# Performance work log

Measured on AMD Instinct MI355X. Metric: run time of the kernel, lower is better.

The kernel has to match this reference:

```python
import jax, jax.numpy as jnp
import numpy as np

B, S, HID, H = 2, 2048, 1024, 16
D_HEAD = HID // H  # 64
EPS = 1e-5


def _gammas():
    lo, hi = np.log(1.0 / 512.0), np.log(1.0 / 32.0)
    return (1.0 - np.exp(np.linspace(lo, hi, H))).astype(np.float32)


def _decay_mask():
    # D[h, n, m] = gamma_h^(n-m) for n >= m else 0  (causal exponential decay)
    gam = jnp.asarray(_gammas())                      # [H]
    pos = jnp.arange(S, dtype=jnp.float32)
    diff = pos[:, None] - pos[None, :]                # [S, S]
    keep = diff >= 0
    logg = jnp.log(gam)[:, None, None]                # [H,1,1]
    safe = jnp.where(keep, diff, 0.0)[None]           # avoid inf for masked entries
    return jnp.where(keep[None], jnp.exp(safe * logg), 0.0)  # [H, S, S]


def setup_inputs() -> dict:
    key = jax.random.key(0)
    ks = jax.random.split(key, 10)
    rn = lambda k, shape, s=1.0: jax.random.normal(k, shape, dtype=jnp.float32) * s
    return {
        "x": rn(ks[0], (B, S, HID)),
        "wq": rn(ks[1], (H, D_HEAD, D_HEAD), 1.0 / np.sqrt(D_HEAD)),
        "bq": rn(ks[2], (H, D_HEAD), 0.02),
        "wk": rn(ks[3], (H, D_HEAD, D_HEAD), 1.0 / np.sqrt(D_HEAD)),
        "bk": rn(ks[4], (H, D_HEAD), 0.02),
        "wv": rn(ks[5], (H, D_HEAD, D_HEAD), 1.0 / np.sqrt(D_HEAD)),
        "theta": rn(ks[6], (H, D_HEAD), 1.0 / D_HEAD),
        "gn_weight": jnp.ones((HID,), jnp.float32),
        "gn_bias": jnp.zeros((HID,), jnp.float32),
        "weight1": rn(ks[7], (HID, HID), 1.0 / HID),
        "weight2": rn(ks[8], (HID, HID), 1.0 / HID),
    }


def reference(x, wq, bq, wk, bk, wv, theta, gn_weight, gn_bias, weight1, weight2):
    # Per-head retention (all heads vectorized; torch loops over heads).
    xh = x.reshape(B, S, H, D_HEAD)
    q = jnp.einsum('bshd,hde->bshe', xh, wq) + bq
    k = jnp.einsum('bshd,hde->bshe', xh, wk) + bk
    v = jnp.einsum('bshd,hde->bshe', xh, wv)
    # Complex rotary factors exp(i*n*theta) on q, conj on k -> real part of q k^H:
    ang = jnp.arange(S, dtype=jnp.float32)[:, None, None] * theta[None]  # [S,H,d]
    cs, sn = jnp.cos(ang), jnp.sin(ang)
    scores = (jnp.einsum('bshd,bthd->bhst', q * cs, k * cs)
              + jnp.einsum('bshd,bthd->bhst', q * sn, k * sn))  # Re(QK^H) [B,H,S,S]
    scores = scores * _decay_mask()[None]                        # decay mask
    ret = jnp.einsum('bhst,bthd->bshd', scores, v)               # [B,S,H,d]
    # GroupNorm with groups = n_heads over channels (per-head normalization).
    mean = jnp.mean(ret, axis=-1, keepdims=True)
    var = jnp.var(ret, axis=-1, keepdims=True)
    retn = (ret - mean) * jax.lax.rsqrt(var + EPS)
    retn = retn.reshape(B, S, HID) * gn_weight + gn_bias
    # Swish gate on x @ W1, residual add, project with W2.
    gate = x @ weight1
    out = gate * jax.nn.sigmoid(gate) + retn
    return out @ weight2
```

## Files before the change

kernel.cpp:

```cpp
#include <hip/hip_runtime.h>
#include <cstdint>
#include <cstddef>

#define B_ 2
#define S_ 2048
#define HID_ 1024
#define H_ 16
#define DH_ 64

typedef __attribute__((ext_vector_type(8))) short short8;
typedef __attribute__((ext_vector_type(8))) unsigned short ushort8;
typedef __attribute__((ext_vector_type(4))) unsigned short ushort4v;
typedef __attribute__((ext_vector_type(4))) float floatx4;
typedef __attribute__((ext_vector_type(4))) float float4v;

static __device__ __forceinline__ unsigned short f2bf(float f) {
  unsigned int u = __float_as_uint(f);
  u += 0x7fffu + ((u >> 16) & 1u);
  return (unsigned short)(u >> 16);
}
static __device__ __forceinline__ float bf2f(unsigned short h) {
  return __uint_as_float(((unsigned int)h) << 16);
}

__global__ __launch_bounds__(256) void convert_kernel(
    const float* __restrict__ x, const float* __restrict__ w1,
    const float* __restrict__ w2, unsigned short* __restrict__ x_bf,
    unsigned short* __restrict__ w1t, unsigned short* __restrict__ w2t_hi,
    unsigned short* __restrict__ w2t_lo) {
  const int NX = B_ * S_ * HID_;
  const int NW = HID_ * HID_;
  int idx = blockIdx.x * 256 + threadIdx.x;
  if (idx < NX) {
    x_bf[idx] = f2bf(x[idx]);
  } else if (idx < NX + NW) {
    int i = idx - NX;
    int n = i >> 10, k = i & 1023;
    w1t[i] = f2bf(w1[k * HID_ + n]);
  } else if (idx < NX + 2 * NW) {
    int i = idx - NX - NW;
    int n = i >> 10, k = i & 1023;
    float v = w2[k * HID_ + n];
    unsigned short h = f2bf(v);
    w2t_hi[i] = h;
    w2t_lo[i] = f2bf(v - bf2f(h));
  }
}

__global__ __launch_bounds__(256) void qkv_kernel(
    const float* __restrict__ x, const float* __restrict__ wq,
    const float* __restrict__ bq, const float* __restrict__ wk,
    const float* __restrict__ bk, const float* __restrict__ wv,
    const float* __restrict__ theta, float* __restrict__ q_f,
    unsigned short* __restrict__ k_h, unsigned short* __restrict__ k_l,
    unsigned short* __restrict__ v_th, unsigned short* __restrict__ v_tl,
    int b) {
  __shared__ __align__(16) float xs[64 * 68];
  __shared__ __align__(16) float wqs[64 * 68];
  __shared__ __align__(16) float wks[64 * 68];
  __shared__ __align__(16) float wvs[64 * 68];

  int tid = threadIdx.x;
  int st = blockIdx.x, h = blockIdx.y;
  int s0 = st * 64;

#pragma unroll
  for (int i = 0; i < 4; ++i) {
    int cid = tid + i * 256;
    int r = cid >> 4, c4 = (cid & 15) * 4;
    *reinterpret_cast<float4v*>(&xs[r * 68 + c4]) =
        *reinterpret_cast<const float4v*>(x + ((size_t)(b * S_ + s0 + r)) * HID_ + h * DH_ + c4);
  }
#pragma unroll
  for (int i = 0; i < 4; ++i) {
    int cid = tid + i * 256;
    int d = cid >> 4, c4 = (cid & 15) * 4;
    *reinterpret_cast<float4v*>(&wqs[d * 68 + c4]) =
        *reinterpret_cast<const float4v*>(wq + (size_t)(h * DH_ + d) * DH_ + c4);
    *reinterpret_cast<float4v*>(&wks[d * 68 + c4]) =
        *reinterpret_cast<const float4v*>(wk + (size_t)(h * DH_ + d) * DH_ + c4);
    *reinterpret_cast<float4v*>(&wvs[d * 68 + c4]) =
        *reinterpret_cast<const float4v*>(wv + (size_t)(h * DH_ + d) * DH_ + c4);
  }
  __syncthreads();

  int rg = tid >> 3;
  int cg = tid & 7;
  int r0 = rg * 2, c0 = cg * 8;

  float aq[2][8], ak[2][8], av[2][8];
#pragma unroll
  for (int i = 0; i < 2; ++i)
#pragma unroll
    for (int j = 0; j < 8; ++j) { aq[i][j] = 0.f; ak[i][j] = 0.f; av[i][j] = 0.f; }

  for (int d = 0; d < 64; ++d) {
    float x0 = xs[(r0 + 0) * 68 + d];
    float x1 = xs[(r0 + 1) * 68 + d];
#pragma unroll
    for (int j = 0; j < 8; ++j) {
      float wqv = wqs[d * 68 + c0 + j];
      float wkv = wks[d * 68 + c0 + j];
      float wvv = wvs[d * 68 + c0 + j];
      aq[0][j] += x0 * wqv; aq[1][j] += x1 * wqv;
      ak[0][j] += x0 * wkv; ak[1][j] += x1 * wkv;
      av[0][j] += x0 * wvv; av[1][j] += x1 * wvv;
    }
  }

  float thv[8], bqv[8], bkv[8];
#pragma unroll
  for (int j = 0; j < 8; ++j) {
    thv[j] = theta[h * DH_ + c0 + j];
    bqv[j] = bq[h * DH_ + c0 + j];
    bkv[j] = bk[h * DH_ + c0 + j];
  }

  __syncthreads();
  unsigned short* VtH = reinterpret_cast<unsigned short*>(xs);
  unsigned short* VtL = reinterpret_cast<unsigned short*>(wqs);

#pragma unroll
  for (int i = 0; i < 2; ++i) {
    int s = s0 + r0 + i;
    size_t qb = ((size_t)h * S_ + s) * 128;
    ushort8 kch, kcl, ksh, ksl;
#pragma unroll
    for (int j = 0; j < 8; ++j) {
      float q = aq[i][j] + bqv[j];
      float k = ak[i][j] + bkv[j];
      float ang = (float)s * thv[j];
      float cs = cosf(ang), sn = sinf(ang);
      q_f[qb + c0 + j] = q * cs;
      q_f[qb + 64 + c0 + j] = q * sn;
      float kc = k * cs, ksn = k * sn;
      unsigned short h1 = f2bf(kc);
      kch[j] = h1;
      kcl[j] = f2bf(kc - bf2f(h1));
      unsigned short h2 = f2bf(ksn);
      ksh[j] = h2;
      ksl[j] = f2bf(ksn - bf2f(h2));
      float vv = av[i][j];
      unsigned short vh1 = f2bf(vv);
      VtH[(c0 + j) * 72 + (r0 + i)] = vh1;
      VtL[(c0 + j) * 72 + (r0 + i)] = f2bf(vv - bf2f(vh1));
    }
    *reinterpret_cast<ushort8*>(k_h + qb + c0) = kch;
    *reinterpret_cast<ushort8*>(k_h + qb + 64 + c0) = ksh;
    *reinterpret_cast<ushort8*>(k_l + qb + c0) = kcl;
    *reinterpret_cast<ushort8*>(k_l + qb + 64 + c0) = ksl;
  }
  __syncthreads();
#pragma unroll
  for (int i = 0; i < 2; ++i) {
    int cid = tid + i * 256;
    int d = cid >> 3, t8 = (cid & 7) * 8;
    size_t gb = ((size_t)(h * 64 + d)) * S_ + s0 + t8;
    *reinterpret_cast<ushort8*>(v_th + gb) = *reinterpret_cast<const ushort8*>(&VtH[d * 72 + t8]);
    *reinterpret_cast<ushort8*>(v_tl + gb) = *reinterpret_cast<const ushort8*>(&VtL[d * 72 + t8]);
  }
}

__global__ __launch_bounds__(256) void retention_fold_kernel(
    const float* __restrict__ q_f, const unsigned short* __restrict__ k_h,
    const unsigned short* __restrict__ k_l,
    const unsigned short* __restrict__ v_th,
    const unsigned short* __restrict__ v_tl, const float* __restrict__ gn_w,
    const float* __restrict__ gn_b, float* __restrict__ retn, int b) {
  __shared__ __align__(16) unsigned short Kh[2][64 * 136];
  __shared__ __align__(16) unsigned short Kl[2][64 * 136];
  __shared__ __align__(16) unsigned short Vh[2][64 * 72];
  __shared__ __align__(16) unsigned short Vl[2][64 * 72];
  __shared__ __align__(16) float Sc[64 * 68];
  __shared__ float gnred[64][8];

  int tid = threadIdx.x;
  int w = tid >> 6;
  int lane = tid & 63, ln = lane & 15, quad = lane >> 4;
  int qp = blockIdx.x, h = blockIdx.y;
  int prow = quad * 4;

  const float lo_c = -6.2383246250395075f, hi_c = -3.4657359027997265f;
  float gam = 1.f - __expf(lo_c + (hi_c - lo_c) * ((float)h * (1.f / 15.f)));
  float logg = __logf(gam);

  float rowf[4], colf[4];
#pragma unroll
  for (int rr = 0; rr < 4; ++rr)
    rowf[rr] = __expf((float)(w * 16 + prow + rr) * logg);
#pragma unroll
  for (int ns = 0; ns < 4; ++ns)
    colf[ns] = __expf(-(float)(ns * 16 + ln) * logg);

  const unsigned short* khb = k_h + (size_t)h * S_ * 128;
  const unsigned short* klb = k_l + (size_t)h * S_ * 128;
  const unsigned short* vhb = v_th + (size_t)h * 64 * S_;
  const unsigned short* vlb = v_tl + (size_t)h * 64 * S_;

  for (int pass = 0; pass < 2; ++pass) {
    int qt = pass ? (31 - qp) : qp;
    int s0 = qt * 64;

    int sQ = s0 + w * 16 + ln;
    const float* qrow = q_f + ((size_t)h * S_ + sQ) * 128 + quad * 8;
    short8 qh[4], ql[4];
#pragma unroll
    for (int c = 0; c < 4; ++c) {
#pragma unroll
      for (int j = 0; j < 8; ++j) {
        float qv = qrow[c * 32 + j];
        unsigned short hh = f2bf(qv);
        qh[c][j] = (short)hh;
        ql[c][j] = (short)f2bf(qv - bf2f(hh));
      }
    }

    floatx4 accO[4];
#pragma unroll
    for (int i = 0; i < 4; ++i) accO[i] = (floatx4){0.f, 0.f, 0.f, 0.f};

    __syncthreads();
#pragma unroll
    for (int i = 0; i < 4; ++i) {
      int cid = tid + i * 256;
      int r = cid >> 4, c8 = (cid & 15) * 8;
      *reinterpret_cast<ushort8*>(&Kh[0][r * 136 + c8]) =
          *reinterpret_cast<const ushort8*>(khb + (size_t)r * 128 + c8);
      *reinterpret_cast<ushort8*>(&Kl[0][r * 136 + c8]) =
          *reinterpret_cast<const ushort8*>(klb + (size_t)r * 128 + c8);
    }
#pragma unroll
    for (int i = 0; i < 2; ++i) {
      int cid = tid + i * 256;
      int d = cid >> 3, t8 = (cid & 7) * 8;
      *reinterpret_cast<ushort8*>(&Vh[0][d * 72 + t8]) =
          *reinterpret_cast<const ushort8*>(vhb + (size_t)d * S_ + t8);
      *reinterpret_cast<ushort8*>(&Vl[0][d * 72 + t8]) =
          *reinterpret_cast<const ushort8*>(vlb + (size_t)d * S_ + t8);
    }

    for (int kt = 0; kt <= qt; ++kt) {
      int cur = kt & 1;
      __syncthreads();

      ushort8 skh[4], skl[4], svh[2], svl[2];
      if (kt < qt) {
        int t0n = (kt + 1) * 64;
#pragma unroll
        for (int i = 0; i < 4; ++i) {
          int cid = tid + i * 256;
          int r = cid >> 4, c8 = (cid & 15) * 8;
          skh[i] = *reinterpret_cast<const ushort8*>(khb + ((size_t)(t0n + r)) * 128 + c8);
          skl[i] = *reinterpret_cast<const ushort8*>(klb + ((size_t)(t0n + r)) * 128 + c8);
        }
#pragma unroll
        for (int i = 0; i < 2; ++i) {
          int cid = tid + i * 256;
          int d = cid >> 3, t8 = (cid & 7) * 8;
          svh[i] = *reinterpret_cast<const ushort8*>(vhb + (size_t)d * S_ + t0n + t8);
          svl[i] = *reinterpret_cast<const ushort8*>(vlb + (size_t)d * S_ + t0n + t8);
        }
      }

      floatx4 accS[4];
#pragma unroll
      for (int ns = 0; ns < 4; ++ns) {
        floatx4 a = (floatx4){0.f, 0.f, 0.f, 0.f};
#pragma unroll
        for (int ks = 0; ks < 4; ++ks) {
          int off = (ns * 16 + ln) * 136 + ks * 32 + quad * 8;
          short8 kh = *reinterpret_cast<const short8*>(&Kh[cur][off]);
          short8 kl = *reinterpret_cast<const short8*>(&Kl[cur][off]);
          a = __builtin_amdgcn_mfma_f32_16x16x32_bf16(qh[ks], kh, a, 0, 0, 0);
          a = __builtin_amdgcn_mfma_f32_16x16x32_bf16(ql[ks], kh, a, 0, 0, 0);
          a = __builtin_amdgcn_mfma_f32_16x16x32_bf16(qh[ks], kl, a, 0, 0, 0);
        }
        accS[ns] = a;
      }

      float tf = __expf((float)(64 * (qt - kt)) * logg);
      float trf[4];
#pragma unroll
      for (int rr = 0; rr < 4; ++rr) trf[rr] = tf * rowf[rr];
      if (kt < qt) {
#pragma unroll
        for (int ns = 0; ns < 4; ++ns)
#pragma unroll
          for (int rr = 0; rr < 4; ++rr)
            Sc[(w * 16 + prow + rr) * 68 + ns * 16 + ln] =
                accS[ns][rr] * trf[rr] * colf[ns];
      } else {
#pragma unroll
        for (int ns = 0; ns < 4; ++ns) {
          int col = ns * 16 + ln;
#pragma unroll
          for (int rr = 0; rr < 4; ++rr) {
            int row = w * 16 + prow + rr;
            float v = accS[ns][rr] * trf[rr] * colf[ns];
            Sc[row * 68 + col] = (row >= col) ? v : 0.f;
          }
        }
      }

      if (kt < qt) {
        int nx = cur ^ 1;
#pragma unroll
        for (int i = 0; i < 4; ++i) {
          int cid = tid + i * 256;
          int r = cid >> 4, c8 = (cid & 15) * 8;
          *reinterpret_cast<ushort8*>(&Kh[nx][r * 136 + c8]) = skh[i];
          *reinterpret_cast<ushort8*>(&Kl[nx][r * 136 + c8]) = skl[i];
        }
#pragma unroll
        for (int i = 0; i < 2; ++i) {
          int cid = tid + i * 256;
          int d = cid >> 3, t8 = (cid & 7) * 8;
          *reinterpret_cast<ushort8*>(&Vh[nx][d * 72 + t8]) = svh[i];
          *reinterpret_cast<ushort8*>(&Vl[nx][d * 72 + t8]) = svl[i];
        }
      }

#pragma unroll
      for (int ks = 0; ks < 2; ++ks) {
        const float* prow_p = &Sc[(w * 16 + ln) * 68 + ks * 32 + quad * 8];
        short8 ph, pl;
#pragma unroll
        for (int j = 0; j < 8; ++j) {
          float pv = prow_p[j];
          unsigned short hh = f2bf(pv);
          ph[j] = (short)hh;
          pl[j] = (short)f2bf(pv - bf2f(hh));
        }
#pragma unroll
        for (int ds = 0; ds < 4; ++ds) {
          int voff = (ds * 16 + ln) * 72 + ks * 32 + quad * 8;
          short8 vh = *reinterpret_cast<const short8*>(&Vh[cur][voff]);
          short8 vl = *reinterpret_cast<const short8*>(&Vl[cur][voff]);
          accO[ds] = __builtin_amdgcn_mfma_f32_16x16x32_bf16(ph, vh, accO[ds], 0, 0, 0);
          accO[ds] = __builtin_amdgcn_mfma_f32_16x16x32_bf16(pl, vh, accO[ds], 0, 0, 0);
          accO[ds] = __builtin_amdgcn_mfma_f32_16x16x32_bf16(ph, vl, accO[ds], 0, 0, 0);
        }
      }
    }

#pragma unroll
    for (int ds = 0; ds < 4; ++ds)
#pragma unroll
      for (int rr = 0; rr < 4; ++rr)
        Sc[(w * 16 + quad * 4 + rr) * 68 + ds * 16 + ln] = accO[ds][rr];

    int r2 = tid >> 2;
    int sub = tid & 3;
    float a16[16];
#pragma unroll
    for (int i = 0; i < 16; ++i) a16[i] = Sc[r2 * 68 + sub * 16 + i];

    float psum = 0.f, psq = 0.f;
#pragma unroll
    for (int i = 0; i < 16; ++i) { psum += a16[i]; psq += a16[i] * a16[i]; }
    gnred[r2][sub] = psum;
    gnred[r2][4 + sub] = psq;
    float sum = gnred[r2][0] + gnred[r2][1] + gnred[r2][2] + gnred[r2][3];
    float sq = gnred[r2][4] + gnred[r2][5] + gnred[r2][6] + gnred[r2][7];
    float mean = sum * (1.f / 64.f);
    float var = sq * (1.f / 64.f) - mean * mean;
    float rstd = rsqrtf(var + 1e-5f);

    size_t obase = ((size_t)(b * S_ + s0 + r2)) * HID_ + h * DH_ + sub * 16;
#pragma unroll
    for (int i = 0; i < 16; ++i) {
      float gw = gn_w[h * DH_ + sub * 16 + i];
      float gb = gn_b[h * DH_ + sub * 16 + i];
      retn[obase + i] = (a16[i] - mean) * rstd * gw + gb;
    }
  }
}

__global__ __launch_bounds__(256) void gemm_gate_kernel(
    const unsigned short* __restrict__ A, const unsigned short* __restrict__ Bt,
    const float* __restrict__ retn, unsigned short* __restrict__ pre_hi,
    unsigned short* __restrict__ pre_lo) {
  const int K = HID_;
  __shared__ __align__(16) unsigned short Al[128 * 56];
  __shared__ __align__(16) unsigned short Bl[128 * 56];

  int tid = threadIdx.x;
  int lane = tid & 63, ln = lane & 15, quad = lane >> 4;
  int w = tid >> 6, wm = w >> 1, wn = w & 1;
  int m0 = blockIdx.y * 128, n0 = blockIdx.x * 128;

  floatx4 acc[4][4];
#pragma unroll
  for (int i = 0; i < 4; ++i)
#pragma unroll
    for (int j = 0; j < 4; ++j) acc[i][j] = (floatx4){0.f, 0.f, 0.f, 0.f};

  for (int k0 = 0; k0 < K; k0 += 32) {
    __syncthreads();
#pragma unroll
    for (int i = 0; i < 2; ++i) {
      int cid = tid + i * 256;
      int r = cid >> 2, c8 = (cid & 3) * 8;
      *reinterpret_cast<ushort8*>(&Al[r * 56 + c8]) =
          *reinterpret_cast<const ushort8*>(A + (size_t)(m0 + r) * K + k0 + c8);
      *reinterpret_cast<ushort8*>(&Bl[r * 56 + c8]) =
          *reinterpret_cast<const ushort8*>(Bt + (size_t)(n0 + r) * K + k0 + c8);
    }
    __syncthreads();

    short8 af[4], bfr[4];
#pragma unroll
    for (int i = 0; i < 4; ++i) {
      af[i] = *reinterpret_cast<const short8*>(&Al[(wm * 64 + i * 16 + ln) * 56 + quad * 8]);
      bfr[i] = *reinterpret_cast<const short8*>(&Bl[(wn * 64 + i * 16 + ln) * 56 + quad * 8]);
    }
#pragma unroll
    for (int mi = 0; mi < 4; ++mi)
#pragma unroll
      for (int ni = 0; ni < 4; ++ni)
        acc[mi][ni] = __builtin_amdgcn_mfma_f32_16x16x32_bf16(af[mi], bfr[ni], acc[mi][ni], 0, 0, 0);
  }

#pragma unroll
  for (int mi = 0; mi < 4; ++mi) {
#pragma unroll
    for (int r = 0; r < 4; ++r) {
      int row = m0 + wm * 64 + mi * 16 + quad * 4 + r;
#pragma unroll
      for (int ni = 0; ni < 4; ++ni) {
        int col = n0 + wn * 64 + ni * 16 + ln;
        float g = acc[mi][ni][r];
        float val = g * (1.f / (1.f + __expf(-g))) + retn[(size_t)row * HID_ + col];
        unsigned short hh = f2bf(val);
        size_t oidx = (size_t)row * HID_ + col;
        pre_hi[oidx] = hh;
        pre_lo[oidx] = f2bf(val - bf2f(hh));
      }
    }
  }
}

__global__ __launch_bounds__(256) void gemm_out_kernel(
    const unsigned short* __restrict__ Ah, const unsigned short* __restrict__ Alo,
    const unsigned short* __restrict__ Bth, const unsigned short* __restrict__ Btlo,
    float* __restrict__ out_f) {
  const int K = HID_;
  __shared__ __align__(16) unsigned short AhS[128 * 56];
  __shared__ __align__(16) unsigned short AlS[128 * 56];
  __shared__ __align__(16) unsigned short BhS[128 * 56];
  __shared__ __align__(16) unsigned short BlS[128 * 56];

  int tid = threadIdx.x;
  int lane = tid & 63, ln = lane & 15, quad = lane >> 4;
  int w = tid >> 6, wm = w >> 1, wn = w & 1;
  int m0 = blockIdx.y * 128, n0 = blockIdx.x * 128;

  floatx4 acc[4][4];
#pragma unroll
  for (int i = 0; i < 4; ++i)
#pragma unroll
    for (int j = 0; j < 4; ++j) acc[i][j] = (floatx4){0.f, 0.f, 0.f, 0.f};

  for (int k0 = 0; k0 < K; k0 += 32) {
    __syncthreads();
#pragma unroll
    for (int i = 0; i < 2; ++i) {
      int cid = tid + i * 256;
      int r = cid >> 2, c8 = (cid & 3) * 8;
      size_t ga = (size_t)(m0 + r) * K + k0 + c8;
      size_t gb = (size_t)(n0 + r) * K + k0 + c8;
      *reinterpret_cast<ushort8*>(&AhS[r * 56 + c8]) = *reinterpret_cast<const ushort8*>(Ah + ga);
      *reinterpret_cast<ushort8*>(&AlS[r * 56 + c8]) = *reinterpret_cast<const ushort8*>(Alo + ga);
      *reinterpret_cast<ushort8*>(&BhS[r * 56 + c8]) = *reinterpret_cast<const ushort8*>(Bth + gb);
      *reinterpret_cast<ushort8*>(&BlS[r * 56 + c8]) = *reinterpret_cast<const ushort8*>(Btlo + gb);
    }
    __syncthreads();

    short8 afh[4], afl[4], bfh[4], bfl[4];
#pragma unroll
    for (int i = 0; i < 4; ++i) {
      int ao = (wm * 64 + i * 16 + ln) * 56 + quad * 8;
      int bo = (wn * 64 + i * 16 + ln) * 56 + quad * 8;
      afh[i] = *reinterpret_cast<const short8*>(&AhS[ao]);
      afl[i] = *reinterpret_cast<const short8*>(&AlS[ao]);
      bfh[i] = *reinterpret_cast<const short8*>(&BhS[bo]);
      bfl[i] = *reinterpret_cast<const short8*>(&BlS[bo]);
    }
#pragma unroll
    for (int mi = 0; mi < 4; ++mi)
#pragma unroll
      for (int ni = 0; ni < 4; ++ni) {
        floatx4 a = acc[mi][ni];
        a = __builtin_amdgcn_mfma_f32_16x16x32_bf16(afh[mi], bfh[ni], a, 0, 0, 0);
        a = __builtin_amdgcn_mfma_f32_16x16x32_bf16(afl[mi], bfh[ni], a, 0, 0, 0);
        a = __builtin_amdgcn_mfma_f32_16x16x32_bf16(afh[mi], bfl[ni], a, 0, 0, 0);
        acc[mi][ni] = a;
      }
  }

#pragma unroll
  for (int mi = 0; mi < 4; ++mi) {
#pragma unroll
    for (int r = 0; r < 4; ++r) {
      int row = m0 + wm * 64 + mi * 16 + quad * 4 + r;
#pragma unroll
      for (int ni = 0; ni < 4; ++ni) {
        int col = n0 + wn * 64 + ni * 16 + ln;
        out_f[(size_t)row * HID_ + col] = acc[mi][ni][r];
      }
    }
  }
}

extern "C" void kernel_launch(void* const* d_in, const int* in_sizes, int n_in,
                              void* d_out, int out_size, void* d_ws,
                              size_t ws_size, hipStream_t stream) {
  (void)in_sizes; (void)n_in; (void)out_size; (void)ws_size;
  const float* x = (const float*)d_in[0];
  const float* wq = (const float*)d_in[1];
  const float* bq = (const float*)d_in[2];
  const float* wk = (const float*)d_in[3];
  const float* bk = (const float*)d_in[4];
  const float* wv = (const float*)d_in[5];
  const float* theta = (const float*)d_in[6];
  const float* gn_w = (const float*)d_in[7];
  const float* gn_b = (const float*)d_in[8];
  const float* w1 = (const float*)d_in[9];
  const float* w2 = (const float*)d_in[10];

  const size_t MB = 1024 * 1024;
  char* ws = (char*)d_ws;
  unsigned short* x_bf   = (unsigned short*)(ws + 0 * MB);
  unsigned short* w1t    = (unsigned short*)(ws + 8 * MB);
  unsigned short* w2t_hi = (unsigned short*)(ws + 10 * MB);
  unsigned short* w2t_lo = (unsigned short*)(ws + 12 * MB);
  float*          q_f    = (float*)(ws + 14 * MB);
  unsigned short* k_h    = (unsigned short*)(ws + 30 * MB);
  unsigned short* k_l    = (unsigned short*)(ws + 38 * MB);
  unsigned short* v_th   = (unsigned short*)(ws + 46 * MB);
  unsigned short* v_tl   = (unsigned short*)(ws + 50 * MB);
  float*          retn   = (float*)(ws + 54 * MB);
  unsigned short* pre_hi = (unsigned short*)(ws + 14 * MB);
  unsigned short* pre_lo = (unsigned short*)(ws + 22 * MB);
  float* out = (float*)d_out;

  convert_kernel<<<dim3(24576), 256, 0, stream>>>(x, w1, w2, x_bf, w1t, w2t_hi, w2t_lo);
  for (int b = 0; b < B_; ++b) {
    qkv_kernel<<<dim3(S_ / 64, H_), 256, 0, stream>>>(
        x, wq, bq, wk, bk, wv, theta, q_f, k_h, k_l, v_th, v_tl, b);
    retention_fold_kernel<<<dim3(16, H_), 256, 0, stream>>>(
        q_f, k_h, k_l, v_th, v_tl, gn_w, gn_b, retn, b);
  }
  gemm_gate_kernel<<<dim3(HID_ / 128, (B_ * S_) / 128), 256, 0, stream>>>(
      x_bf, w1t, retn, pre_hi, pre_lo);
  gemm_out_kernel<<<dim3(HID_ / 128, (B_ * S_) / 128), 256, 0, stream>>>(
      pre_hi, pre_lo, w2t_hi, w2t_lo, out);
}
```

Baseline: 372.0 us.

## Pre-split Q into bf16 hi/lo, XOR-swizzle LDS tiles, remap retention grid

The qkv kernel now writes Q as bf16 hi/lo pairs, so the retention kernel no longer reads fp32 Q and splits it per element. The retention kernel's K, V and score tiles drop row padding in shared memory and use an XOR swizzle to avoid bank conflicts, with vectorized float4 reads of scores. The grid is flattened to 256 blocks and blockIdx is remapped so that heads are interleaved across blocks, which changes the order work is dispatched. The swizzle adds index arithmetic, and the Q workspace layout changes.

```diff
diff --git a/kernel.cpp b/kernel.cpp
--- a/kernel.cpp
+++ b/kernel.cpp
@@ -51,7 +51,8 @@
     const float* __restrict__ x, const float* __restrict__ wq,
     const float* __restrict__ bq, const float* __restrict__ wk,
     const float* __restrict__ bk, const float* __restrict__ wv,
-    const float* __restrict__ theta, float* __restrict__ q_f,
+    const float* __restrict__ theta,
+    unsigned short* __restrict__ q_h, unsigned short* __restrict__ q_l,
     unsigned short* __restrict__ k_h, unsigned short* __restrict__ k_l,
     unsigned short* __restrict__ v_th, unsigned short* __restrict__ v_tl,
     int b) {
@@ -124,15 +125,20 @@
   for (int i = 0; i < 2; ++i) {
     int s = s0 + r0 + i;
     size_t qb = ((size_t)h * S_ + s) * 128;
-    ushort8 kch, kcl, ksh, ksl;
+    ushort8 qch, qcl, qsh, qsl, kch, kcl, ksh, ksl;
 #pragma unroll
     for (int j = 0; j < 8; ++j) {
       float q = aq[i][j] + bqv[j];
       float k = ak[i][j] + bkv[j];
       float ang = (float)s * thv[j];
       float cs = cosf(ang), sn = sinf(ang);
-      q_f[qb + c0 + j] = q * cs;
-      q_f[qb + 64 + c0 + j] = q * sn;
+      float qc = q * cs, qs = q * sn;
+      unsigned short hq1 = f2bf(qc);
+      qch[j] = hq1;
+      qcl[j] = f2bf(qc - bf2f(hq1));
+      unsigned short hq2 = f2bf(qs);
+      qsh[j] = hq2;
+      qsl[j] = f2bf(qs - bf2f(hq2));
       float kc = k * cs, ksn = k * sn;
       unsigned short h1 = f2bf(kc);
       kch[j] = h1;
@@ -145,6 +151,10 @@
       VtH[(c0 + j) * 72 + (r0 + i)] = vh1;
       VtL[(c0 + j) * 72 + (r0 + i)] = f2bf(vv - bf2f(vh1));
     }
+    *reinterpret_cast<ushort8*>(q_h + qb + c0) = qch;
+    *reinterpret_cast<ushort8*>(q_h + qb + 64 + c0) = qsh;
+    *reinterpret_cast<ushort8*>(q_l + qb + c0) = qcl;
+    *reinterpret_cast<ushort8*>(q_l + qb + 64 + c0) = qsl;
     *reinterpret_cast<ushort8*>(k_h + qb + c0) = kch;
     *reinterpret_cast<ushort8*>(k_h + qb + 64 + c0) = ksh;
     *reinterpret_cast<ushort8*>(k_l + qb + c0) = kcl;
@@ -161,23 +171,35 @@
   }
 }
 
+#define KOFF(buf, row, cu) ((buf) * 16384 + (row) * 256 + ((((cu) * 2)) ^ (((row) & 7) << 4)))
+#define VOFF(buf, d, tu)   ((buf) * 8192 + (d) * 128 + ((((tu) * 2)) ^ (((d) & 7) << 4)))
+#define SCOFF(row, colb)   ((row) * 256 + ((colb) ^ (((row) & 7) << 4)))
+
 __global__ __launch_bounds__(256) void retention_fold_kernel(
-    const float* __restrict__ q_f, const unsigned short* __restrict__ k_h,
-    const unsigned short* __restrict__ k_l,
-    const unsigned short* __restrict__ v_th,
-    const unsigned short* __restrict__ v_tl, const float* __restrict__ gn_w,
-    const float* __restrict__ gn_b, float* __restrict__ retn, int b) {
-  __shared__ __align__(16) unsigned short Kh[2][64 * 136];
-  __shared__ __align__(16) unsigned short Kl[2][64 * 136];
-  __shared__ __align__(16) unsigned short Vh[2][64 * 72];
-  __shared__ __align__(16) unsigned short Vl[2][64 * 72];
-  __shared__ __align__(16) float Sc[64 * 68];
+    const unsigned short* __restrict__ q_h, const unsigned short* __restrict__ q_l,
+    const unsigned short* __restrict__ k_h, const unsigned short* __restrict__ k_l,
+    const unsigned short* __restrict__ v_th, const unsigned short* __restrict__ v_tl,
+    const float* __restrict__ gn_w, const float* __restrict__ gn_b,
+    float* __restrict__ retn, int b) {
+  __shared__ __align__(16) unsigned short Kh[2][64 * 128];
+  __shared__ __align__(16) unsigned short Kl[2][64 * 128];
+  __shared__ __align__(16) unsigned short Vh[2][64 * 64];
+  __shared__ __align__(16) unsigned short Vl[2][64 * 64];
+  __shared__ __align__(16) float Sc[64 * 64];
   __shared__ float gnred[64][8];
+
+  char* KhB = (char*)Kh;
+  char* KlB = (char*)Kl;
+  char* VhB = (char*)Vh;
+  char* VlB = (char*)Vl;
+  char* ScB = (char*)Sc;
 
   int tid = threadIdx.x;
   int w = tid >> 6;
   int lane = tid & 63, ln = lane & 15, quad = lane >> 4;
-  int qp = blockIdx.x, h = blockIdx.y;
+  int f = blockIdx.x;
+  int h = ((f & 7) << 1) | ((f >> 7) & 1);
+  int qp = (f >> 3) & 15;
   int prow = quad * 4;
 
   const float lo_c = -6.2383246250395075f, hi_c = -3.4657359027997265f;
@@ -202,17 +224,13 @@
     int s0 = qt * 64;
 
     int sQ = s0 + w * 16 + ln;
-    const float* qrow = q_f + ((size_t)h * S_ + sQ) * 128 + quad * 8;
-    short8 qh[4], ql[4];
+    const unsigned short* qhp = q_h + ((size_t)h * S_ + sQ) * 128 + quad * 8;
+    const unsigned short* qlp = q_l + ((size_t)h * S_ + sQ) * 128 + quad * 8;
+    short8 qfh[4], qfl[4];
 #pragma unroll
     for (int c = 0; c < 4; ++c) {
-#pragma unroll
-      for (int j = 0; j < 8; ++j) {
-        float qv = qrow[c * 32 + j];
-        unsigned short hh = f2bf(qv);
-        qh[c][j] = (short)hh;
-        ql[c][j] = (short)f2bf(qv - bf2f(hh));
-      }
+      qfh[c] = *reinterpret_cast<const short8*>(qhp + c * 32);
+      qfl[c] = *reinterpret_cast<const short8*>(qlp + c * 32);
     }
 
     floatx4 accO[4];
@@ -224,18 +242,20 @@
     for (int i = 0; i < 4; ++i) {
       int cid = tid + i * 256;
       int r = cid >> 4, c8 = (cid & 15) * 8;
-      *reinterpret_cast<ushort8*>(&Kh[0][r * 136 + c8]) =
+      int ko = KOFF(0, r, c8);
+      *reinterpret_cast<ushort8*>(KhB + ko) =
           *reinterpret_cast<const ushort8*>(khb + (size_t)r * 128 + c8);
-      *reinterpret_cast<ushort8*>(&Kl[0][r * 136 + c8]) =
+      *reinterpret_cast<ushort8*>(KlB + ko) =
           *reinterpret_cast<const ushort8*>(klb + (size_t)r * 128 + c8);
     }
 #pragma unroll
     for (int i = 0; i < 2; ++i) {
       int cid = tid + i * 256;
       int d = cid >> 3, t8 = (cid & 7) * 8;
-      *reinterpret_cast<ushort8*>(&Vh[0][d * 72 + t8]) =
+      int vo = VOFF(0, d, t8);
+      *reinterpret_cast<ushort8*>(VhB + vo) =
           *reinterpret_cast<const ushort8*>(vhb + (size_t)d * S_ + t8);
-      *reinterpret_cast<ushort8*>(&Vl[0][d * 72 + t8]) =
+      *reinterpret_cast<ushort8*>(VlB + vo) =
           *reinterpret_cast<const ushort8*>(vlb + (size_t)d * S_ + t8);
     }
 
@@ -266,14 +286,15 @@
 #pragma unroll
       for (int ns = 0; ns < 4; ++ns) {
         floatx4 a = (floatx4){0.f, 0.f, 0.f, 0.f};
+        int row = ns * 16 + ln;
 #pragma unroll
         for (int ks = 0; ks < 4; ++ks) {
-          int off = (ns * 16 + ln) * 136 + ks * 32 + quad * 8;
-          short8 kh = *reinterpret_cast<const short8*>(&Kh[cur][off]);
-          short8 kl = *reinterpret_cast<const short8*>(&Kl[cur][off]);
-          a = __builtin_amdgcn_mfma_f32_16x16x32_bf16(qh[ks], kh, a, 0, 0, 0);
-          a = __builtin_amdgcn_mfma_f32_16x16x32_bf16(ql[ks], kh, a, 0, 0, 0);
-          a = __builtin_amdgcn_mfma_f32_16x16x32_bf16(qh[ks], kl, a, 0, 0, 0);
+          int off = cur * 16384 + row * 256 + ((ks * 64 + quad * 16) ^ ((ln & 7) << 4));
+          short8 kh = *reinterpret_cast<const short8*>(KhB + off);
+          short8 kl = *reinterpret_cast<const short8*>(KlB + off);
+          a = __builtin_amdgcn_mfma_f32_16x16x32_bf16(qfh[ks], kh, a, 0, 0, 0);
+          a = __builtin_amdgcn_mfma_f32_16x16x32_bf16(qfl[ks], kh, a, 0, 0, 0);
+          a = __builtin_amdgcn_mfma_f32_16x16x32_bf16(qfh[ks], kl, a, 0, 0, 0);
         }
         accS[ns] = a;
       }
@@ -284,11 +305,15 @@
       for (int rr = 0; rr < 4; ++rr) trf[rr] = tf * rowf[rr];
       if (kt < qt) {
 #pragma unroll
-        for (int ns = 0; ns < 4; ++ns)
-#pragma unroll
-          for (int rr = 0; rr < 4; ++rr)
-            Sc[(w * 16 + prow + rr) * 68 + ns * 16 + ln] =
+        for (int ns = 0; ns < 4; ++ns) {
+          int col = ns * 16 + ln;
+#pragma unroll
+          for (int rr = 0; rr < 4; ++rr) {
+            int row = w * 16 + prow + rr;
+            *reinterpret_cast<float*>(ScB + SCOFF(row, col * 4)) =
                 accS[ns][rr] * trf[rr] * colf[ns];
+          }
+        }
       } else {
 #pragma unroll
         for (int ns = 0; ns < 4; ++ns) {
@@ -297,7 +322,8 @@
           for (int rr = 0; rr < 4; ++rr) {
             int row = w * 16 + prow + rr;
             float v = accS[ns][rr] * trf[rr] * colf[ns];
-            Sc[row * 68 + col] = (row >= col) ? v : 0.f;
+            *reinterpret_cast<float*>(ScB + SCOFF(row, col * 4)) =
+                (row >= col) ? v : 0.f;
           }
         }
       }
@@ -308,34 +334,42 @@
         for (int i = 0; i < 4; ++i) {
           int cid = tid + i * 256;
           int r = cid >> 4, c8 = (cid & 15) * 8;
-          *reinterpret_cast<ushort8*>(&Kh[nx][r * 136 + c8]) = skh[i];
-          *reinterpret_cast<ushort8*>(&Kl[nx][r * 136 + c8]) = skl[i];
+          int ko = KOFF(nx, r, c8);
+          *reinterpret_cast<ushort8*>(KhB + ko) = skh[i];
+          *reinterpret_cast<ushort8*>(KlB + ko) = skl[i];
         }
 #pragma unroll
         for (int i = 0; i < 2; ++i) {
           int cid = tid + i * 256;
           int d = cid >> 3, t8 = (cid & 7) * 8;
-          *reinterpret_cast<ushort8*>(&Vh[nx][d * 72 + t8]) = svh[i];
-          *reinterpret_cast<ushort8*>(&Vl[nx][d * 72 + t8]) = svl[i];
+          int vo = VOFF(nx, d, t8);
+          *reinterpret_cast<ushort8*>(VhB + vo) = svh[i];
+          *reinterpret_cast<ushort8*>(VlB + vo) = svl[i];
         }
       }
 
 #pragma unroll
       for (int ks = 0; ks < 2; ++ks) {
-        const float* prow_p = &Sc[(w * 16 + ln) * 68 + ks * 32 + quad * 8];
+        int prw = w * 16 + ln;
+        int cb = ks * 128 + quad * 32;
+        float4v p0 = *reinterpret_cast<const float4v*>(ScB + SCOFF(prw, cb));
+        float4v p1 = *reinterpret_cast<const float4v*>(ScB + SCOFF(prw, cb + 16));
         short8 ph, pl;
 #pragma unroll
-        for (int j = 0; j < 8; ++j) {
-          float pv = prow_p[j];
-          unsigned short hh = f2bf(pv);
+        for (int j = 0; j < 4; ++j) {
+          unsigned short hh = f2bf(p0[j]);
           ph[j] = (short)hh;
-          pl[j] = (short)f2bf(pv - bf2f(hh));
+          pl[j] = (short)f2bf(p0[j] - bf2f(hh));
+          unsigned short hh2 = f2bf(p1[j]);
+          ph[4 + j] = (short)hh2;
+          pl[4 + j] = (short)f2bf(p1[j] - bf2f(hh2));
         }
 #pragma unroll
         for (int ds = 0; ds < 4; ++ds) {
-          int voff = (ds * 16 + ln) * 72 + ks * 32 + quad * 8;
-          short8 vh = *reinterpret_cast<const short8*>(&Vh[cur][voff]);
-          short8 vl = *reinterpret_cast<const short8*>(&Vl[cur][voff]);
+          int d = ds * 16 + ln;
+          int voff = cur * 8192 + d * 128 + ((ks * 64 + quad * 16) ^ ((ln & 7) << 4));
+          short8 vh = *reinterpret_cast<const short8*>(VhB + voff);
+          short8 vl = *reinterpret_cast<const short8*>(VlB + voff);
           accO[ds] = __builtin_amdgcn_mfma_f32_16x16x32_bf16(ph, vh, accO[ds], 0, 0, 0);
           accO[ds] = __builtin_amdgcn_mfma_f32_16x16x32_bf16(pl, vh, accO[ds], 0, 0, 0);
           accO[ds] = __builtin_amdgcn_mfma_f32_16x16x32_bf16(ph, vl, accO[ds], 0, 0, 0);
@@ -344,16 +378,23 @@
     }
 
 #pragma unroll
-    for (int ds = 0; ds < 4; ++ds)
-#pragma unroll
-      for (int rr = 0; rr < 4; ++rr)
-        Sc[(w * 16 + quad * 4 + rr) * 68 + ds * 16 + ln] = accO[ds][rr];
+    for (int ds = 0; ds < 4; ++ds) {
+#pragma unroll
+      for (int rr = 0; rr < 4; ++rr) {
+        int row = w * 16 + quad * 4 + rr;
+        *reinterpret_cast<float*>(ScB + SCOFF(row, (ds * 16 + ln) * 4)) = accO[ds][rr];
+      }
+    }
 
     int r2 = tid >> 2;
     int sub = tid & 3;
     float a16[16];
 #pragma unroll
-    for (int i = 0; i < 16; ++i) a16[i] = Sc[r2 * 68 + sub * 16 + i];
+    for (int c = 0; c < 4; ++c) {
+      float4v t = *reinterpret_cast<const float4v*>(ScB + SCOFF(r2, sub * 64 + c * 16));
+#pragma unroll
+      for (int j = 0; j < 4; ++j) a16[c * 4 + j] = t[j];
+    }
 
     float psum = 0.f, psq = 0.f;
 #pragma unroll
@@ -534,7 +575,8 @@
   unsigned short* w1t    = (unsigned short*)(ws + 8 * MB);
   unsigned short* w2t_hi = (unsigned short*)(ws + 10 * MB);
   unsigned short* w2t_lo = (unsigned short*)(ws + 12 * MB);
-  float*          q_f    = (float*)(ws + 14 * MB);
+  unsigned short* q_h    = (unsigned short*)(ws + 14 * MB);
+  unsigned short* q_l    = (unsigned short*)(ws + 22 * MB);
   unsigned short* k_h    = (unsigned short*)(ws + 30 * MB);
   unsigned short* k_l    = (unsigned short*)(ws + 38 * MB);
   unsigned short* v_th   = (unsigned short*)(ws + 46 * MB);
@@ -547,9 +589,9 @@
   convert_kernel<<<dim3(24576), 256, 0, stream>>>(x, w1, w2, x_bf, w1t, w2t_hi, w2t_lo);
   for (int b = 0; b < B_; ++b) {
     qkv_kernel<<<dim3(S_ / 64, H_), 256, 0, stream>>>(
-        x, wq, bq, wk, bk, wv, theta, q_f, k_h, k_l, v_th, v_tl, b);
-    retention_fold_kernel<<<dim3(16, H_), 256, 0, stream>>>(
-        q_f, k_h, k_l, v_th, v_tl, gn_w, gn_b, retn, b);
+        x, wq, bq, wk, bk, wv, theta, q_h, q_l, k_h, k_l, v_th, v_tl, b);
+    retention_fold_kernel<<<dim3(256), 256, 0, stream>>>(
+        q_h, q_l, k_h, k_l, v_th, v_tl, gn_w, gn_b, retn, b);
   }
   gemm_gate_kernel<<<dim3(HID_ / 128, (B_ * S_) / 128), 256, 0, stream>>>(
       x_bf, w1t, retn, pre_hi, pre_lo);
```

After: 397.7 us. 6.9% more time.
